# Kernel optimization log

Hardware: AMD Instinct MI355X
Metric: run time of the kernel (lower is better)

Reference implementation:

```python
import jax, jax.numpy as jnp
import numpy as np

EPS = 1e-5
DELTA = 0.2
VIS_LAM = 1.0


def setup_inputs() -> dict:
    key = jax.random.key(0)
    k1, k2, k3 = jax.random.split(key, 3)
    Na, Ns, Nb, Ne, D = 16, 32, 100, 12, 512
    vis_feats = jax.random.normal(k1, (Na * Ns * Nb, D), dtype=jnp.float32)
    word_feats = jax.random.normal(k2, (Na * Ne, D), dtype=jnp.float32)
    entities_length = jax.random.randint(k3, (Na,), 0, Ne).astype(jnp.int64)
    return {"vis_feats": vis_feats, "word_feats": word_feats,
            "entities_length": entities_length, "Nb": Nb}


def reference(vis_feats, word_feats, entities_length, Nb):
    Na = entities_length.shape[0]
    Ne = word_feats.shape[0] // Na
    Ns = vis_feats.shape[0] // (Na * Nb)
    D = vis_feats.shape[1]
    ent = entities_length

    div_vec = jnp.where(ent == 0, 1, ent).astype(vis_feats.dtype)      # (Na,)
    # pad mask: entity slot e is padding for action a if e >= ent[a]
    col_mask = jnp.arange(Ne)[None, :] >= ent[:, None]                 # (Na, Ne)

    # masked similarity: (Na*Ns*Nb, Na*Ne)
    S_ = vis_feats @ word_feats.T
    S_ = jnp.where(col_mask.reshape(-1)[None, :], 0.0, S_)

    # --- train-only visual consistency loss ---
    S_vt = S_.reshape(Na, Ns, Nb, Na, Ne)
    # diagonal over the two action axes: S_vis[i] = S_vt[i,:,:,i,:]
    S_vis = S_vt[jnp.arange(Na), :, :, jnp.arange(Na), :]              # (Na, Ns, Nb, Ne)
    S_vis_ng = jax.lax.stop_gradient(S_vis)                            # torch.no_grad block
    sim_scr = S_vis_ng.max(axis=2)                                     # (Na, Ns, Ne)
    maxind = jnp.argmax(S_vis_ng, axis=2)                              # (Na, Ns, Ne)
    smin = sim_scr.min(axis=1, keepdims=True)
    smax = sim_scr.max(axis=1, keepdims=True)
    sim_scr = ((sim_scr - smin) / (smax - smin + EPS))[..., None]      # (Na, Ns, Ne, 1)

    # NOTE: original code indexes vis_feats with the raw box index (< Nb);
    # reproduced faithfully.
    vcls = vis_feats[maxind.reshape(-1)].reshape(Na, Ns, Ne, D)
    vcls = vcls / (jnp.linalg.norm(vcls, axis=3, keepdims=True) + EPS)
    vcls = vcls * sim_scr
    v1 = vcls.transpose(0, 2, 1, 3)                                    # (Na, Ne, Ns, D)
    vis_mat = 1.0 - jnp.einsum('aesd,aetd->aest', v1, v1)              # (Na, Ne, Ns, Ns)
    eye = jnp.eye(Ns, dtype=bool)
    mvis = col_mask[:, :, None, None] | eye[None, None, :, :]
    vis_mat = jnp.where(mvis, 0.0, vis_mat)
    dem = jnp.count_nonzero(vis_mat).astype(vis_mat.dtype)
    vis_loss = vis_mat.sum() / dem

    # --- margin loss over frame-level scores ---
    S = S_.reshape(Na * Ns, Nb, Na * Ne).max(axis=1).reshape(Na, Ns, Na * Ne)
    Smin = S.min(axis=1, keepdims=True)
    Smax = S.max(axis=1, keepdims=True)
    S = S * ((S - Smin) / (Smax - Smin + EPS))
    Sf = S.reshape(Na, Ns, Na, Ne).sum(-1) / div_vec                   # (Na, Ns, Na)
    Sf_diag = Sf[jnp.arange(Na), :, jnp.arange(Na)]                    # (Na, Ns)
    term1 = jax.nn.relu(Sf - Sf_diag.T[None, :, :] + DELTA).mean(0).T  # (Na, Ns)
    term2 = jax.nn.relu(Sf - Sf_diag[:, :, None] + DELTA).mean(2)      # (Na, Ns)
    frame_score = term1 + term2
    margin_loss = (frame_score.mean() + VIS_LAM * vis_loss) * 10.0

    S_sim = S_.reshape(Na * Ns, Nb, Na * Ne)
    D_sim = S_sim.max(axis=1)
    D_ind = jnp.argmax(S_sim, axis=1)
    return (D_ind, D_sim, margin_loss)
```

## Files before the change

### kernel.cpp

```cpp
#include <hip/hip_runtime.h>
#include <math.h>

#define NA 16
#define NS 32
#define NB 100
#define NE 12
#define DD 512
#define NQ (NA*NS)
#define NC (NA*NE)
#define OUT_SIM_OFF (NQ*NC)
#define EPSF 1e-5f
#define DELTAF 0.2f
#define EPS_R 0.15f

#define WS_B_FOFF 12288

typedef _Float16 f16x8 __attribute__((ext_vector_type(8)));
typedef float f32x4 __attribute__((ext_vector_type(4)));

__global__ __launch_bounds__(64) void k0_conv(
    const float* __restrict__ word, float* __restrict__ ws)
{
    const int kcc = blockIdx.x / 12;
    const int nt  = blockIdx.x - kcc*12;
    const int l   = threadIdx.x;
    if (blockIdx.x == 0 && l < 2) ws[l] = 0.f;

    const int col = nt*16 + (l & 15);
    const int k   = kcc*32 + (l >> 4)*8;
    const float* src = word + (size_t)col*DD + k;
    float4 v0 = *(const float4*)(src);
    float4 v1 = *(const float4*)(src + 4);
    f16x8 hv;
    hv[0]=(_Float16)v0.x; hv[1]=(_Float16)v0.y; hv[2]=(_Float16)v0.z; hv[3]=(_Float16)v0.w;
    hv[4]=(_Float16)v1.x; hv[5]=(_Float16)v1.y; hv[6]=(_Float16)v1.z; hv[7]=(_Float16)v1.w;
    unsigned short* wsB = (unsigned short*)(ws + WS_B_FOFF);
    const int kc2 = kcc >> 1, ks = kcc & 1;
    *(f16x8*)&wsB[(size_t)(((kc2*12 + nt)*2 + ks)*512) + l*8] = hv;
}

__global__ __launch_bounds__(512, 4) void k1_mfma(
    const float* __restrict__ vis, const float* __restrict__ word,
    const unsigned short* __restrict__ wsB,
    const int* __restrict__ ent, float* __restrict__ out)
{
    __shared__ __align__(16) char pool[81920];
    unsigned short* Abuf = (unsigned short*)pool;
    unsigned short* Bbuf = (unsigned short*)(pool + 32768);
    float* part_v = (float*)pool;
    int*   part_i = (int*)(pool + 1536);
    float* colmax = (float*)(pool + 3072);
    int*   cnts   = (int*)(pool + 3840);
    int*   cand   = (int*)(pool + 4608);
    int*   flist  = (int*)(pool + 5376);
    int*   nflag  = (int*)(pool + 6144);

    const int t    = threadIdx.x;
    const int lane = t & 63;
    const int wid  = t >> 6;
    const int wm   = wid >> 2;
    const int wn   = wid & 3;
    const int q    = blockIdx.x;
    const float* visq = vis + (size_t)q * NB * DD;

    f32x4 acc[4][3];
    #pragma unroll
    for (int mi = 0; mi < 4; mi++)
        #pragma unroll
        for (int ni = 0; ni < 3; ni++) acc[mi][ni] = (f32x4)0.f;

    float4 ar[4];

    #define A_LOAD(kb)                                                         \
        {   int l_ = t & 63;                                                   \
            int row = ((t >> 6) << 4) + (l_ & 15);                             \
            ar[0] = make_float4(0.f,0.f,0.f,0.f); ar[1] = ar[0];               \
            ar[2] = ar[0]; ar[3] = ar[0];                                      \
            if (row < NB) {                                                    \
                const float* p_ = visq + (size_t)row*DD + (kb) + ((l_>>4)<<3); \
                ar[0] = *(const float4*)p_;                                    \
                ar[1] = *(const float4*)(p_ + 4);                              \
                ar[2] = *(const float4*)(p_ + 32);                             \
                ar[3] = *(const float4*)(p_ + 36); } }
    #define A_STORE(pn)                                                       \
        {   int mt_ = t >> 6;                                                 \
            f16x8 h0, h1;                                                     \
            h0[0]=(_Float16)ar[0].x; h0[1]=(_Float16)ar[0].y;                 \
            h0[2]=(_Float16)ar[0].z; h0[3]=(_Float16)ar[0].w;                 \
            h0[4]=(_Float16)ar[1].x; h0[5]=(_Float16)ar[1].y;                 \
            h0[6]=(_Float16)ar[1].z; h0[7]=(_Float16)ar[1].w;                 \
            h1[0]=(_Float16)ar[2].x; h1[1]=(_Float16)ar[2].y;                 \
            h1[2]=(_Float16)ar[2].z; h1[3]=(_Float16)ar[2].w;                 \
            h1[4]=(_Float16)ar[3].x; h1[5]=(_Float16)ar[3].y;                 \
            h1[6]=(_Float16)ar[3].z; h1[7]=(_Float16)ar[3].w;                 \
            *(f16x8*)&Abuf[(pn)*8192 + (mt_*2+0)*512 + (t&63)*8] = h0;        \
            *(f16x8*)&Abuf[(pn)*8192 + (mt_*2+1)*512 + (t&63)*8] = h1; }
    #define B_STAGE(kcn, pn)                                                   \
        {   const unsigned short* bsrc = wsB + (size_t)(kcn)*12288;            \
            unsigned short* bdst = Bbuf + (pn)*12288;                          \
            _Pragma("unroll")                                                  \
            for (int i = 0; i < 3; i++)                                        \
                __builtin_amdgcn_global_load_lds(                              \
                    (const void*)(bsrc + ((size_t)(i*512 + wid*64 + lane))*8), \
                    (void*)(bdst + (i*512 + wid*64)*8), 16, 0, 0); }

    {
        B_STAGE(0, 0);
        A_LOAD(0);
        A_STORE(0);
    }
    __syncthreads();

    for (int kc = 0; kc < 8; ++kc) {
        const int p = kc & 1;
        if (kc < 7) {
            A_LOAD((kc+1)*64);
            B_STAGE(kc+1, p^1);
        }
        {
            const unsigned short* Bp = Bbuf + p*12288;
            const unsigned short* Ap = Abuf + p*8192;
            #pragma unroll
            for (int ks = 0; ks < 2; ks++) {
                f16x8 bf[3];
                #pragma unroll
                for (int ni = 0; ni < 3; ni++)
                    bf[ni] = *((const f16x8*)&Bp[((wn*3 + ni)*2 + ks)*512 + lane*8]);
                #pragma unroll
                for (int mi = 0; mi < 4; mi++) {
                    f16x8 af = *((const f16x8*)&Ap[((wm*4 + mi)*2 + ks)*512 + lane*8]);
                    #pragma unroll
                    for (int ni = 0; ni < 3; ni++)
                        acc[mi][ni] = __builtin_amdgcn_mfma_f32_16x16x32_f16(af, bf[ni], acc[mi][ni], 0, 0, 0);
                }
            }
        }
        if (kc < 7) { A_STORE(p^1); }
        __syncthreads();
    }

    #pragma unroll
    for (int ni = 0; ni < 3; ni++) {
        float bv = -INFINITY; int bg = 1000;
        #pragma unroll
        for (int mi = 0; mi < 4; mi++)
            #pragma unroll
            for (int r = 0; r < 4; r++) {
                int g = wm*64 + mi*16 + ((lane>>4)<<2) + r;
                float v = acc[mi][ni][r];
                if (g < NB && (v > bv || (v == bv && g < bg))) { bv = v; bg = g; }
            }
        #pragma unroll
        for (int off = 16; off <= 32; off <<= 1) {
            float ov = __shfl_xor(bv, off);
            int   og = __shfl_xor(bg, off);
            if (ov > bv || (ov == bv && og < bg)) { bv = ov; bg = og; }
        }
        if (lane < 16) {
            int col = wn*48 + ni*16 + lane;
            part_v[wm*NC + col] = bv; part_i[wm*NC + col] = bg;
        }
    }
    if (t < NC) { cnts[t] = 0; cand[t] = 0; }
    if (t == 0) *nflag = 0;
    __syncthreads();

    float fbv = 0.f; int fbg = 0; bool fmask = true;
    if (t < NC) {
        fbv = part_v[t]; fbg = part_i[t];
        float v1 = part_v[NC + t]; int g1 = part_i[NC + t];
        if (v1 > fbv || (v1 == fbv && g1 < fbg)) { fbv = v1; fbg = g1; }
        int a2 = t / NE, e = t - a2*NE;
        fmask = (e >= ent[a2]);
        colmax[t] = fmask ? INFINITY : fbv;
    }
    __syncthreads();

    #pragma unroll
    for (int ni = 0; ni < 3; ni++) {
        int col = wn*48 + ni*16 + (lane & 15);
        float cm = colmax[col] - EPS_R;
        #pragma unroll
        for (int mi = 0; mi < 4; mi++)
            #pragma unroll
            for (int r = 0; r < 4; r++) {
                int g = wm*64 + mi*16 + ((lane>>4)<<2) + r;
                float v = acc[mi][ni][r];
                if (g < NB && v >= cm) {
                    int s = atomicAdd(&cnts[col], 1);
                    if (s < 3) atomicOr(&cand[col], (g + 1) << (8*s));
                }
            }
    }
    __syncthreads();

    if (t < NC) {
        if (fmask) {
            out[(size_t)q*NC + t] = 0.f;
            out[OUT_SIM_OFF + (size_t)q*NC + t] = 0.f;
        } else if (cnts[t] <= 1) {
            out[(size_t)q*NC + t] = (float)fbg;
            out[OUT_SIM_OFF + (size_t)q*NC + t] = fbv;
        } else {
            int idx = atomicAdd(nflag, 1);
            flist[idx] = t;
        }
    }
    __syncthreads();

    const int nf = *nflag;
    for (int f = wid; f < nf; f += 8) {
        int col = flist[f];
        int cnt = cnts[col];
        const float* wc = word + (size_t)col*DD;
        float bv; int bg;
        if (cnt <= 3) {
            int grp = lane >> 4, li = lane & 15;
            int cpk = cand[col];
            int myrow = (grp < cnt) ? (((cpk >> (8*grp)) & 255) - 1) : -1;
            float d = 0.f;
            if (myrow >= 0) {
                const float* vr = visq + (size_t)myrow*DD + li*32;
                const float* wb = wc + li*32;
                #pragma unroll
                for (int m = 0; m < 8; ++m) {
                    float4 a = *(const float4*)(vr + m*4);
                    float4 b = *(const float4*)(wb + m*4);
                    d = fmaf(a.x, b.x, d); d = fmaf(a.y, b.y, d);
                    d = fmaf(a.z, b.z, d); d = fmaf(a.w, b.w, d);
                }
            }
            #pragma unroll
            for (int off = 1; off <= 8; off <<= 1) d += __shfl_xor(d, off);
            float v0 = __shfl(d, 0), v1 = __shfl(d, 16), v2 = __shfl(d, 32);
            int r0 = ( cpk        & 255) - 1;
            int r1 = ((cpk >> 8)  & 255) - 1;
            int r2 = ((cpk >> 16) & 255) - 1;
            bv = v0; bg = r0;
            if (cnt >= 2 && (v1 > bv || (v1 == bv && r1 < bg))) { bv = v1; bg = r1; }
            if (cnt >= 3 && (v2 > bv || (v2 == bv && r2 < bg))) { bv = v2; bg = r2; }
        } else {
            float mbv = -INFINITY; int mbg = 1000;
            for (int r = lane; r < NB; r += 64) {
                float d = 0.f;
                const float* vr = visq + (size_t)r*DD;
                for (int m = 0; m < DD/4; ++m) {
                    float4 a = *(const float4*)(vr + m*4);
                    float4 b = *(const float4*)(wc + m*4);
                    d = fmaf(a.x, b.x, d); d = fmaf(a.y, b.y, d);
                    d = fmaf(a.z, b.z, d); d = fmaf(a.w, b.w, d);
                }
                if (d > mbv || (d == mbv && r < mbg)) { mbv = d; mbg = r; }
            }
            bv = mbv; bg = mbg;
            #pragma unroll
            for (int off = 32; off >= 1; off >>= 1) {
                float ov = __shfl_xor(bv, off); int og = __shfl_xor(bg, off);
                if (ov > bv || (ov == bv && og < bg)) { bv = ov; bg = og; }
            }
        }
        if (lane == 0) {
            out[(size_t)q*NC + col] = (float)bg;
            out[OUT_SIM_OFF + (size_t)q*NC + col] = bv;
        }
    }
}

__global__ __launch_bounds__(256) void k23_fused(
    const float* __restrict__ vis, const int* __restrict__ ent,
    const float* __restrict__ out_ro, float* __restrict__ ws)
{
    __shared__ __align__(16) char pool[74240];
    const int t = threadIdx.x;

    if (blockIdx.x < 192) {
        const int a = blockIdx.x / NE;
        const int e = blockIdx.x - a*NE;
        if (e >= ent[a]) return;

        float* VT   = (float*)pool;
        float* simv = (float*)(pool + 73728);
        int*   indv = (int*)(pool + 73856);
        float* scl  = (float*)(pool + 73984);
        float* wsum = (float*)(pool + 74112);
        float* wcnt = (float*)(pool + 74128);

        if (t < NS) {
            int q = a*NS + t;
            simv[t] = out_ro[OUT_SIM_OFF + (size_t)q*NC + a*NE + e];
            indv[t] = (int)out_ro[(size_t)q*NC + a*NE + e];
        }
        __syncthreads();
        if (t < NS) {
            float v = simv[t];
            float mn = v, mx = v;
            #pragma unroll
            for (int off = 16; off >= 1; off >>= 1) {
                mn = fminf(mn, __shfl_xor(mn, off));
                mx = fmaxf(mx, __shfl_xor(mx, off));
            }
            simv[t] = (v - mn) / (mx - mn + EPSF);
        }
        __syncthreads();

        const int g = t >> 3, j = t & 7;
        const float* src = vis + (size_t)indv[g]*DD;
        float ss = 0.f;
        #pragma unroll
        for (int i = 0; i < 16; i++) {
            int k4 = j + 8*i;
            float4 v = *(const float4*)(src + k4*4);
            ss = fmaf(v.x,v.x, fmaf(v.y,v.y, fmaf(v.z,v.z, fmaf(v.w,v.w, ss))));
            int k = k4*4;
            VT[(k+0)*36 + g] = v.x;
            VT[(k+1)*36 + g] = v.y;
            VT[(k+2)*36 + g] = v.z;
            VT[(k+3)*36 + g] = v.w;
        }
        #pragma unroll
        for (int off = 4; off >= 1; off >>= 1) ss += __shfl_xor(ss, off);
        if (j == 0) scl[g] = simv[g] / (sqrtf(ss) + EPSF);
        __syncthreads();

        const int s = t >> 3, tq = t & 7;
        float g0=0.f, g1=0.f, g2=0.f, g3=0.f;
        for (int k = 0; k < DD; k++) {
            float vs = VT[k*36 + s];
            float4 vt = *(const float4*)&VT[k*36 + tq*4];
            g0 = fmaf(vs, vt.x, g0);
            g1 = fmaf(vs, vt.y, g1);
            g2 = fmaf(vs, vt.z, g2);
            g3 = fmaf(vs, vt.w, g3);
        }
        float lsum = 0.f, lcnt = 0.f;
        float sc_s = scl[s];
        float gv[4] = {g0, g1, g2, g3};
        #pragma unroll
        for (int jj = 0; jj < 4; jj++) {
            int tt = tq*4 + jj;
            if (tt != s) {
                float val = 1.f - sc_s * scl[tt] * gv[jj];
                lsum += val;
                if (val != 0.f) lcnt += 1.f;
            }
        }
        #pragma unroll
        for (int off = 32; off >= 1; off >>= 1) {
            lsum += __shfl_xor(lsum, off);
            lcnt += __shfl_xor(lcnt, off);
        }
        const int wid = t >> 6, lane = t & 63;
        if (lane == 0) { wsum[wid] = lsum; wcnt[wid] = lcnt; }
        __syncthreads();
        if (t == 0) {
            atomicAdd(&ws[0], wsum[0]+wsum[1]+wsum[2]+wsum[3]);
            atomicAdd(&ws[1], wcnt[0]+wcnt[1]+wcnt[2]+wcnt[3]);
        }
    } else {
        const int a = blockIdx.x - 192;
        float* Ss  = (float*)pool;
        float* Smn = (float*)(pool + 24576);
        float* Smx = (float*)(pool + 25344);

        for (int e2 = t; e2 < NS*NC; e2 += 256) {
            int s = e2 / NC, c = e2 - (e2/NC)*NC;
            Ss[s*NC + c] = out_ro[OUT_SIM_OFF + (size_t)(a*NS + s)*NC + c];
        }
        __syncthreads();
        if (t < NC) {
            float mn = INFINITY, mx = -INFINITY;
            #pragma unroll
            for (int s = 0; s < NS; s++) {
                float v = Ss[s*NC + t];
                mn = fminf(mn, v); mx = fmaxf(mx, v);
            }
            Smn[t] = mn; Smx[t] = mx;
        }
        __syncthreads();
        for (int p = t; p < NS*NA; p += 256) {
            int s = p >> 4, b = p & 15;
            int eb = ent[b];
            float dv = (eb == 0) ? 1.f : (float)eb;
            float sum = 0.f;
            #pragma unroll
            for (int e2 = 0; e2 < NE; e2++) {
                int c = b*NE + e2;
                float S = Ss[s*NC + c];
                float r = (S - Smn[c]) / (Smx[c] - Smn[c] + EPSF);
                sum += S * r;
            }
            ws[2 + a*(NS*NA) + s*NA + b] = sum / dv;
        }
    }
}

__global__ __launch_bounds__(256) void k4_final(
    const float* __restrict__ ws_ro, float* __restrict__ out)
{
    __shared__ float Sf[NA][NS][NA];
    __shared__ float dg[NA][NS];
    __shared__ float wred[4];
    const int t = threadIdx.x;
    for (int e2 = t; e2 < NA*NS*NA; e2 += 256)
        ((float*)Sf)[e2] = ws_ro[2 + e2];
    __syncthreads();
    for (int p = t; p < NA*NS; p += 256) {
        int aa = p >> 5, s = p & 31;
        dg[aa][s] = Sf[aa][s][aa];
    }
    __syncthreads();
    float fsum = 0.f;
    for (int p = t; p < NA*NS; p += 256) {
        int i = p >> 5, s = p & 31;
        float d = dg[i][s];
        float t1 = 0.f, t2 = 0.f;
        #pragma unroll
        for (int x = 0; x < NA; x++) {
            t1 += fmaxf(Sf[x][s][i] - d + DELTAF, 0.f);
            t2 += fmaxf(Sf[i][s][x] - d + DELTAF, 0.f);
        }
        fsum += (t1 + t2) * (1.f/16.f);
    }
    #pragma unroll
    for (int off = 32; off >= 1; off >>= 1) fsum += __shfl_xor(fsum, off);
    const int wid = t >> 6, lane = t & 63;
    if (lane == 0) wred[wid] = fsum;
    __syncthreads();
    if (t == 0) {
        float frame_mean = (wred[0]+wred[1]+wred[2]+wred[3]) / 512.f;
        float vis_loss = ws_ro[0] / ws_ro[1];
        out[2*OUT_SIM_OFF] = (frame_mean + 1.0f * vis_loss) * 10.f;
    }
}

extern "C" void kernel_launch(void* const* d_in, const int* in_sizes, int n_in,
                              void* d_out, int out_size, void* d_ws, size_t ws_size,
                              hipStream_t stream)
{
    (void)in_sizes; (void)n_in; (void)out_size; (void)ws_size;
    const float* vis  = (const float*)d_in[0];
    const float* word = (const float*)d_in[1];
    const int*   ent  = (const int*)d_in[2];
    float* out = (float*)d_out;
    float* ws  = (float*)d_ws;
    const unsigned short* wsB = (const unsigned short*)(ws + WS_B_FOFF);

    k0_conv<<<192, 64, 0, stream>>>(word, ws);
    k1_mfma<<<NQ, 512, 0, stream>>>(vis, word, wsB, ent, out);
    k23_fused<<<208, 256, 0, stream>>>(vis, ent, out, ws);
    k4_final<<<1, 256, 0, stream>>>(ws, out);
}
```

Before: 56.89 us.

## Deepen GEMM A-prefetch pipeline and fold final reduction into last block

```diff
diff --git a/kernel.cpp b/kernel.cpp
--- a/kernel.cpp
+++ b/kernel.cpp
@@ -13,6 +13,7 @@
 #define DELTAF 0.2f
 #define EPS_R 0.15f
 
+#define WS_SF 16
 #define WS_B_FOFF 12288
 
 typedef _Float16 f16x8 __attribute__((ext_vector_type(8)));
@@ -24,7 +25,7 @@
     const int kcc = blockIdx.x / 12;
     const int nt  = blockIdx.x - kcc*12;
     const int l   = threadIdx.x;
-    if (blockIdx.x == 0 && l < 2) ws[l] = 0.f;
+    if (blockIdx.x == 0 && l < 3) ws[l] = 0.f;
 
     const int col = nt*16 + (l & 15);
     const int k   = kcc*32 + (l >> 4)*8;
@@ -69,30 +70,30 @@
         #pragma unroll
         for (int ni = 0; ni < 3; ni++) acc[mi][ni] = (f32x4)0.f;
 
-    float4 ar[4];
-
-    #define A_LOAD(kb)                                                         \
+    float4 arA[4], arB[4];
+
+    #define A_LOAD(dst, kb)                                                    \
         {   int l_ = t & 63;                                                   \
             int row = ((t >> 6) << 4) + (l_ & 15);                             \
-            ar[0] = make_float4(0.f,0.f,0.f,0.f); ar[1] = ar[0];               \
-            ar[2] = ar[0]; ar[3] = ar[0];                                      \
+            dst[0] = make_float4(0.f,0.f,0.f,0.f); dst[1] = dst[0];            \
+            dst[2] = dst[0]; dst[3] = dst[0];                                  \
             if (row < NB) {                                                    \
                 const float* p_ = visq + (size_t)row*DD + (kb) + ((l_>>4)<<3); \
-                ar[0] = *(const float4*)p_;                                    \
-                ar[1] = *(const float4*)(p_ + 4);                              \
-                ar[2] = *(const float4*)(p_ + 32);                             \
-                ar[3] = *(const float4*)(p_ + 36); } }
-    #define A_STORE(pn)                                                       \
+                dst[0] = *(const float4*)p_;                                   \
+                dst[1] = *(const float4*)(p_ + 4);                             \
+                dst[2] = *(const float4*)(p_ + 32);                            \
+                dst[3] = *(const float4*)(p_ + 36); } }
+    #define A_STORE(src, pn)                                                  \
         {   int mt_ = t >> 6;                                                 \
             f16x8 h0, h1;                                                     \
-            h0[0]=(_Float16)ar[0].x; h0[1]=(_Float16)ar[0].y;                 \
-            h0[2]=(_Float16)ar[0].z; h0[3]=(_Float16)ar[0].w;                 \
-            h0[4]=(_Float16)ar[1].x; h0[5]=(_Float16)ar[1].y;                 \
-            h0[6]=(_Float16)ar[1].z; h0[7]=(_Float16)ar[1].w;                 \
-            h1[0]=(_Float16)ar[2].x; h1[1]=(_Float16)ar[2].y;                 \
-            h1[2]=(_Float16)ar[2].z; h1[3]=(_Float16)ar[2].w;                 \
-            h1[4]=(_Float16)ar[3].x; h1[5]=(_Float16)ar[3].y;                 \
-            h1[6]=(_Float16)ar[3].z; h1[7]=(_Float16)ar[3].w;                 \
+            h0[0]=(_Float16)src[0].x; h0[1]=(_Float16)src[0].y;               \
+            h0[2]=(_Float16)src[0].z; h0[3]=(_Float16)src[0].w;               \
+            h0[4]=(_Float16)src[1].x; h0[5]=(_Float16)src[1].y;               \
+            h0[6]=(_Float16)src[1].z; h0[7]=(_Float16)src[1].w;               \
+            h1[0]=(_Float16)src[2].x; h1[1]=(_Float16)src[2].y;               \
+            h1[2]=(_Float16)src[2].z; h1[3]=(_Float16)src[2].w;               \
+            h1[4]=(_Float16)src[3].x; h1[5]=(_Float16)src[3].y;               \
+            h1[6]=(_Float16)src[3].z; h1[7]=(_Float16)src[3].w;               \
             *(f16x8*)&Abuf[(pn)*8192 + (mt_*2+0)*512 + (t&63)*8] = h0;        \
             *(f16x8*)&Abuf[(pn)*8192 + (mt_*2+1)*512 + (t&63)*8] = h1; }
     #define B_STAGE(kcn, pn)                                                   \
@@ -104,18 +105,26 @@
                     (const void*)(bsrc + ((size_t)(i*512 + wid*64 + lane))*8), \
                     (void*)(bdst + (i*512 + wid*64)*8), 16, 0, 0); }
 
-    {
-        B_STAGE(0, 0);
-        A_LOAD(0);
-        A_STORE(0);
-    }
-    __syncthreads();
+    A_LOAD(arA, 0);
+    B_STAGE(0, 0);
+    A_LOAD(arB, 64);
+    A_STORE(arA, 0);
+    asm volatile("s_waitcnt vmcnt(4) lgkmcnt(0)" ::: "memory");
+    __builtin_amdgcn_sched_barrier(0);
+    __builtin_amdgcn_s_barrier();
+    __builtin_amdgcn_sched_barrier(0);
 
     for (int kc = 0; kc < 8; ++kc) {
         const int p = kc & 1;
         if (kc < 7) {
-            A_LOAD((kc+1)*64);
+            if ((kc & 1) == 0) { A_STORE(arB, p^1); } else { A_STORE(arA, p^1); }
             B_STAGE(kc+1, p^1);
+            __builtin_amdgcn_sched_barrier(0);
+            if (kc < 6) {
+                if ((kc & 1) == 0) { A_LOAD(arA, (kc+2)*64); }
+                else               { A_LOAD(arB, (kc+2)*64); }
+            }
+            __builtin_amdgcn_sched_barrier(0);
         }
         {
             const unsigned short* Bp = Bbuf + p*12288;
@@ -135,9 +144,17 @@
                 }
             }
         }
-        if (kc < 7) { A_STORE(p^1); }
-        __syncthreads();
-    }
+        if (kc < 7) {
+            if (kc < 6)
+                asm volatile("s_waitcnt vmcnt(4) lgkmcnt(0)" ::: "memory");
+            else
+                asm volatile("s_waitcnt vmcnt(0) lgkmcnt(0)" ::: "memory");
+            __builtin_amdgcn_sched_barrier(0);
+            __builtin_amdgcn_s_barrier();
+            __builtin_amdgcn_sched_barrier(0);
+        }
+    }
+    __syncthreads();
 
     #pragma unroll
     for (int ni = 0; ni < 3; ni++) {
@@ -268,93 +285,94 @@
 
 __global__ __launch_bounds__(256) void k23_fused(
     const float* __restrict__ vis, const int* __restrict__ ent,
-    const float* __restrict__ out_ro, float* __restrict__ ws)
+    const float* __restrict__ out_ro, float* ws, float* out)
 {
     __shared__ __align__(16) char pool[74240];
+    __shared__ int lastFlag;
     const int t = threadIdx.x;
 
     if (blockIdx.x < 192) {
         const int a = blockIdx.x / NE;
         const int e = blockIdx.x - a*NE;
-        if (e >= ent[a]) return;
-
-        float* VT   = (float*)pool;
-        float* simv = (float*)(pool + 73728);
-        int*   indv = (int*)(pool + 73856);
-        float* scl  = (float*)(pool + 73984);
-        float* wsum = (float*)(pool + 74112);
-        float* wcnt = (float*)(pool + 74128);
-
-        if (t < NS) {
-            int q = a*NS + t;
-            simv[t] = out_ro[OUT_SIM_OFF + (size_t)q*NC + a*NE + e];
-            indv[t] = (int)out_ro[(size_t)q*NC + a*NE + e];
-        }
-        __syncthreads();
-        if (t < NS) {
-            float v = simv[t];
-            float mn = v, mx = v;
-            #pragma unroll
-            for (int off = 16; off >= 1; off >>= 1) {
-                mn = fminf(mn, __shfl_xor(mn, off));
-                mx = fmaxf(mx, __shfl_xor(mx, off));
-            }
-            simv[t] = (v - mn) / (mx - mn + EPSF);
-        }
-        __syncthreads();
-
-        const int g = t >> 3, j = t & 7;
-        const float* src = vis + (size_t)indv[g]*DD;
-        float ss = 0.f;
-        #pragma unroll
-        for (int i = 0; i < 16; i++) {
-            int k4 = j + 8*i;
-            float4 v = *(const float4*)(src + k4*4);
-            ss = fmaf(v.x,v.x, fmaf(v.y,v.y, fmaf(v.z,v.z, fmaf(v.w,v.w, ss))));
-            int k = k4*4;
-            VT[(k+0)*36 + g] = v.x;
-            VT[(k+1)*36 + g] = v.y;
-            VT[(k+2)*36 + g] = v.z;
-            VT[(k+3)*36 + g] = v.w;
-        }
-        #pragma unroll
-        for (int off = 4; off >= 1; off >>= 1) ss += __shfl_xor(ss, off);
-        if (j == 0) scl[g] = simv[g] / (sqrtf(ss) + EPSF);
-        __syncthreads();
-
-        const int s = t >> 3, tq = t & 7;
-        float g0=0.f, g1=0.f, g2=0.f, g3=0.f;
-        for (int k = 0; k < DD; k++) {
-            float vs = VT[k*36 + s];
-            float4 vt = *(const float4*)&VT[k*36 + tq*4];
-            g0 = fmaf(vs, vt.x, g0);
-            g1 = fmaf(vs, vt.y, g1);
-            g2 = fmaf(vs, vt.z, g2);
-            g3 = fmaf(vs, vt.w, g3);
-        }
-        float lsum = 0.f, lcnt = 0.f;
-        float sc_s = scl[s];
-        float gv[4] = {g0, g1, g2, g3};
-        #pragma unroll
-        for (int jj = 0; jj < 4; jj++) {
-            int tt = tq*4 + jj;
-            if (tt != s) {
-                float val = 1.f - sc_s * scl[tt] * gv[jj];
-                lsum += val;
-                if (val != 0.f) lcnt += 1.f;
-            }
-        }
-        #pragma unroll
-        for (int off = 32; off >= 1; off >>= 1) {
-            lsum += __shfl_xor(lsum, off);
-            lcnt += __shfl_xor(lcnt, off);
-        }
-        const int wid = t >> 6, lane = t & 63;
-        if (lane == 0) { wsum[wid] = lsum; wcnt[wid] = lcnt; }
-        __syncthreads();
-        if (t == 0) {
-            atomicAdd(&ws[0], wsum[0]+wsum[1]+wsum[2]+wsum[3]);
-            atomicAdd(&ws[1], wcnt[0]+wcnt[1]+wcnt[2]+wcnt[3]);
+        if (e < ent[a]) {
+            float* VT   = (float*)pool;
+            float* simv = (float*)(pool + 73728);
+            int*   indv = (int*)(pool + 73856);
+            float* scl  = (float*)(pool + 73984);
+            float* wsum = (float*)(pool + 74112);
+            float* wcnt = (float*)(pool + 74128);
+
+            if (t < NS) {
+                int q = a*NS + t;
+                simv[t] = out_ro[OUT_SIM_OFF + (size_t)q*NC + a*NE + e];
+                indv[t] = (int)out_ro[(size_t)q*NC + a*NE + e];
+            }
+            __syncthreads();
+            if (t < NS) {
+                float v = simv[t];
+                float mn = v, mx = v;
+                #pragma unroll
+                for (int off = 16; off >= 1; off >>= 1) {
+                    mn = fminf(mn, __shfl_xor(mn, off));
+                    mx = fmaxf(mx, __shfl_xor(mx, off));
+                }
+                simv[t] = (v - mn) / (mx - mn + EPSF);
+            }
+            __syncthreads();
+
+            const int g = t >> 3, j = t & 7;
+            const float* src = vis + (size_t)indv[g]*DD;
+            float ss = 0.f;
+            #pragma unroll
+            for (int i = 0; i < 16; i++) {
+                int k4 = j + 8*i;
+                float4 v = *(const float4*)(src + k4*4);
+                ss = fmaf(v.x,v.x, fmaf(v.y,v.y, fmaf(v.z,v.z, fmaf(v.w,v.w, ss))));
+                int k = k4*4;
+                VT[(k+0)*36 + g] = v.x;
+                VT[(k+1)*36 + g] = v.y;
+                VT[(k+2)*36 + g] = v.z;
+                VT[(k+3)*36 + g] = v.w;
+            }
+            #pragma unroll
+            for (int off = 4; off >= 1; off >>= 1) ss += __shfl_xor(ss, off);
+            if (j == 0) scl[g] = simv[g] / (sqrtf(ss) + EPSF);
+            __syncthreads();
+
+            const int s = t >> 3, tq = t & 7;
+            float g0=0.f, g1=0.f, g2=0.f, g3=0.f;
+            for (int k = 0; k < DD; k++) {
+                float vs = VT[k*36 + s];
+                float4 vt = *(const float4*)&VT[k*36 + tq*4];
+                g0 = fmaf(vs, vt.x, g0);
+                g1 = fmaf(vs, vt.y, g1);
+                g2 = fmaf(vs, vt.z, g2);
+                g3 = fmaf(vs, vt.w, g3);
+            }
+            float lsum = 0.f, lcnt = 0.f;
+            float sc_s = scl[s];
+            float gv[4] = {g0, g1, g2, g3};
+            #pragma unroll
+            for (int jj = 0; jj < 4; jj++) {
+                int tt = tq*4 + jj;
+                if (tt != s) {
+                    float val = 1.f - sc_s * scl[tt] * gv[jj];
+                    lsum += val;
+                    if (val != 0.f) lcnt += 1.f;
+                }
+            }
+            #pragma unroll
+            for (int off = 32; off >= 1; off >>= 1) {
+                lsum += __shfl_xor(lsum, off);
+                lcnt += __shfl_xor(lcnt, off);
+            }
+            const int wid = t >> 6, lane = t & 63;
+            if (lane == 0) { wsum[wid] = lsum; wcnt[wid] = lcnt; }
+            __syncthreads();
+            if (t == 0) {
+                atomicAdd(&ws[0], wsum[0]+wsum[1]+wsum[2]+wsum[3]);
+                atomicAdd(&ws[1], wcnt[0]+wcnt[1]+wcnt[2]+wcnt[3]);
+            }
         }
     } else {
         const int a = blockIdx.x - 192;
@@ -389,47 +407,51 @@
                 float r = (S - Smn[c]) / (Smx[c] - Smn[c] + EPSF);
                 sum += S * r;
             }
-            ws[2 + a*(NS*NA) + s*NA + b] = sum / dv;
-        }
-    }
-}
-
-__global__ __launch_bounds__(256) void k4_final(
-    const float* __restrict__ ws_ro, float* __restrict__ out)
-{
-    __shared__ float Sf[NA][NS][NA];
-    __shared__ float dg[NA][NS];
-    __shared__ float wred[4];
-    const int t = threadIdx.x;
-    for (int e2 = t; e2 < NA*NS*NA; e2 += 256)
-        ((float*)Sf)[e2] = ws_ro[2 + e2];
-    __syncthreads();
-    for (int p = t; p < NA*NS; p += 256) {
-        int aa = p >> 5, s = p & 31;
-        dg[aa][s] = Sf[aa][s][aa];
-    }
-    __syncthreads();
-    float fsum = 0.f;
-    for (int p = t; p < NA*NS; p += 256) {
-        int i = p >> 5, s = p & 31;
-        float d = dg[i][s];
-        float t1 = 0.f, t2 = 0.f;
+            ws[WS_SF + a*(NS*NA) + s*NA + b] = sum / dv;
+        }
+    }
+
+    __threadfence();
+    if (t == 0) {
+        unsigned old = atomicAdd((unsigned int*)(ws + 2), 1u);
+        lastFlag = (old == 207u) ? 1 : 0;
+    }
+    __syncthreads();
+    if (lastFlag) {
+        __threadfence();
+        float* Sf   = (float*)pool;
+        float* dg   = (float*)(pool + 32768);
+        float* wred = (float*)(pool + 34816);
+        for (int e2 = t; e2 < NA*NS*NA; e2 += 256)
+            Sf[e2] = ws[WS_SF + e2];
+        __syncthreads();
+        for (int p = t; p < NA*NS; p += 256) {
+            int aa = p >> 5, s = p & 31;
+            dg[aa*NS + s] = Sf[(aa*NS + s)*NA + aa];
+        }
+        __syncthreads();
+        float fsum = 0.f;
+        for (int p = t; p < NA*NS; p += 256) {
+            int i = p >> 5, s = p & 31;
+            float d = dg[i*NS + s];
+            float t1 = 0.f, t2 = 0.f;
+            #pragma unroll
+            for (int x = 0; x < NA; x++) {
+                t1 += fmaxf(Sf[(x*NS + s)*NA + i] - d + DELTAF, 0.f);
+                t2 += fmaxf(Sf[(i*NS + s)*NA + x] - d + DELTAF, 0.f);
+            }
+            fsum += (t1 + t2) * (1.f/16.f);
+        }
         #pragma unroll
-        for (int x = 0; x < NA; x++) {
-            t1 += fmaxf(Sf[x][s][i] - d + DELTAF, 0.f);
-            t2 += fmaxf(Sf[i][s][x] - d + DELTAF, 0.f);
-        }
-        fsum += (t1 + t2) * (1.f/16.f);
-    }
-    #pragma unroll
-    for (int off = 32; off >= 1; off >>= 1) fsum += __shfl_xor(fsum, off);
-    const int wid = t >> 6, lane = t & 63;
-    if (lane == 0) wred[wid] = fsum;
-    __syncthreads();
-    if (t == 0) {
-        float frame_mean = (wred[0]+wred[1]+wred[2]+wred[3]) / 512.f;
-        float vis_loss = ws_ro[0] / ws_ro[1];
-        out[2*OUT_SIM_OFF] = (frame_mean + 1.0f * vis_loss) * 10.f;
+        for (int off = 32; off >= 1; off >>= 1) fsum += __shfl_xor(fsum, off);
+        const int wid = t >> 6, lane = t & 63;
+        if (lane == 0) wred[wid] = fsum;
+        __syncthreads();
+        if (t == 0) {
+            float frame_mean = (wred[0]+wred[1]+wred[2]+wred[3]) / 512.f;
+            float vis_loss = ws[0] / ws[1];
+            out[2*OUT_SIM_OFF] = (frame_mean + 1.0f * vis_loss) * 10.f;
+        }
     }
 }
 
@@ -447,6 +469,5 @@
 
     k0_conv<<<192, 64, 0, stream>>>(word, ws);
     k1_mfma<<<NQ, 512, 0, stream>>>(vis, word, wsB, ent, out);
-    k23_fused<<<208, 256, 0, stream>>>(vis, ent, out, ws);
-    k4_final<<<1, 256, 0, stream>>>(ws, out);
+    k23_fused<<<208, 256, 0, stream>>>(vis, ent, out, ws, out);
 }
```

Result: slower. 66.95 us (+17.7%).

## Load A fragments directly into registers and give each wave all columns

Applied to the files above, without the earlier changes.

```diff
diff --git a/kernel.cpp b/kernel.cpp
--- a/kernel.cpp
+++ b/kernel.cpp
@@ -44,112 +44,92 @@
     const unsigned short* __restrict__ wsB,
     const int* __restrict__ ent, float* __restrict__ out)
 {
-    __shared__ __align__(16) char pool[81920];
-    unsigned short* Abuf = (unsigned short*)pool;
-    unsigned short* Bbuf = (unsigned short*)(pool + 32768);
+    __shared__ __align__(16) char pool[49152];
+    unsigned short* Bbuf = (unsigned short*)pool;
     float* part_v = (float*)pool;
-    int*   part_i = (int*)(pool + 1536);
-    float* colmax = (float*)(pool + 3072);
-    int*   cnts   = (int*)(pool + 3840);
-    int*   cand   = (int*)(pool + 4608);
-    int*   flist  = (int*)(pool + 5376);
-    int*   nflag  = (int*)(pool + 6144);
+    int*   part_i = (int*)(pool + 6144);
+    float* colmax = (float*)(pool + 12288);
+    int*   cnts   = (int*)(pool + 13056);
+    int*   cand   = (int*)(pool + 13824);
+    int*   flist  = (int*)(pool + 14592);
+    int*   nflag  = (int*)(pool + 15360);
 
     const int t    = threadIdx.x;
     const int lane = t & 63;
-    const int wid  = t >> 6;
-    const int wm   = wid >> 2;
-    const int wn   = wid & 3;
+    const int w    = t >> 6;
     const int q    = blockIdx.x;
     const float* visq = vis + (size_t)q * NB * DD;
 
-    f32x4 acc[4][3];
+    f32x4 acc[12];
     #pragma unroll
-    for (int mi = 0; mi < 4; mi++)
-        #pragma unroll
-        for (int ni = 0; ni < 3; ni++) acc[mi][ni] = (f32x4)0.f;
-
-    float4 ar[4];
-
-    #define A_LOAD(kb)                                                         \
-        {   int l_ = t & 63;                                                   \
-            int row = ((t >> 6) << 4) + (l_ & 15);                             \
-            ar[0] = make_float4(0.f,0.f,0.f,0.f); ar[1] = ar[0];               \
-            ar[2] = ar[0]; ar[3] = ar[0];                                      \
-            if (row < NB) {                                                    \
-                const float* p_ = visq + (size_t)row*DD + (kb) + ((l_>>4)<<3); \
-                ar[0] = *(const float4*)p_;                                    \
-                ar[1] = *(const float4*)(p_ + 4);                              \
-                ar[2] = *(const float4*)(p_ + 32);                             \
-                ar[3] = *(const float4*)(p_ + 36); } }
-    #define A_STORE(pn)                                                       \
-        {   int mt_ = t >> 6;                                                 \
-            f16x8 h0, h1;                                                     \
-            h0[0]=(_Float16)ar[0].x; h0[1]=(_Float16)ar[0].y;                 \
-            h0[2]=(_Float16)ar[0].z; h0[3]=(_Float16)ar[0].w;                 \
-            h0[4]=(_Float16)ar[1].x; h0[5]=(_Float16)ar[1].y;                 \
-            h0[6]=(_Float16)ar[1].z; h0[7]=(_Float16)ar[1].w;                 \
-            h1[0]=(_Float16)ar[2].x; h1[1]=(_Float16)ar[2].y;                 \
-            h1[2]=(_Float16)ar[2].z; h1[3]=(_Float16)ar[2].w;                 \
-            h1[4]=(_Float16)ar[3].x; h1[5]=(_Float16)ar[3].y;                 \
-            h1[6]=(_Float16)ar[3].z; h1[7]=(_Float16)ar[3].w;                 \
-            *(f16x8*)&Abuf[(pn)*8192 + (mt_*2+0)*512 + (t&63)*8] = h0;        \
-            *(f16x8*)&Abuf[(pn)*8192 + (mt_*2+1)*512 + (t&63)*8] = h1; }
+    for (int nt = 0; nt < 12; nt++) acc[nt] = (f32x4)0.f;
+
+    int arow = w*16 + (lane & 15);
+    const float* aptr = visq + (size_t)(arow < NB ? arow : 0)*DD + ((lane >> 4) << 3);
+
     #define B_STAGE(kcn, pn)                                                   \
         {   const unsigned short* bsrc = wsB + (size_t)(kcn)*12288;            \
             unsigned short* bdst = Bbuf + (pn)*12288;                          \
             _Pragma("unroll")                                                  \
             for (int i = 0; i < 3; i++)                                        \
                 __builtin_amdgcn_global_load_lds(                              \
-                    (const void*)(bsrc + ((size_t)(i*512 + wid*64 + lane))*8), \
-                    (void*)(bdst + (i*512 + wid*64)*8), 16, 0, 0); }
-
+                    (const void*)(bsrc + ((size_t)(i*512 + w*64 + lane))*8),   \
+                    (void*)(bdst + (i*512 + w*64)*8), 16, 0, 0); }
+
+    float4 ar[2][4];
+
+    B_STAGE(0, 0);
     {
-        B_STAGE(0, 0);
-        A_LOAD(0);
-        A_STORE(0);
-    }
-    __syncthreads();
-
+        const float* p_ = aptr;
+        ar[0][0] = *(const float4*)(p_);
+        ar[0][1] = *(const float4*)(p_ + 4);
+        ar[0][2] = *(const float4*)(p_ + 32);
+        ar[0][3] = *(const float4*)(p_ + 36);
+    }
+    __syncthreads();
+
+    #pragma unroll
     for (int kc = 0; kc < 8; ++kc) {
         const int p = kc & 1;
         if (kc < 7) {
-            A_LOAD((kc+1)*64);
             B_STAGE(kc+1, p^1);
-        }
+            const float* p_ = aptr + (kc+1)*64;
+            ar[p^1][0] = *(const float4*)(p_);
+            ar[p^1][1] = *(const float4*)(p_ + 4);
+            ar[p^1][2] = *(const float4*)(p_ + 32);
+            ar[p^1][3] = *(const float4*)(p_ + 36);
+        }
+        f16x8 af0, af1;
+        af0[0]=(_Float16)ar[p][0].x; af0[1]=(_Float16)ar[p][0].y;
+        af0[2]=(_Float16)ar[p][0].z; af0[3]=(_Float16)ar[p][0].w;
+        af0[4]=(_Float16)ar[p][1].x; af0[5]=(_Float16)ar[p][1].y;
+        af0[6]=(_Float16)ar[p][1].z; af0[7]=(_Float16)ar[p][1].w;
+        af1[0]=(_Float16)ar[p][2].x; af1[1]=(_Float16)ar[p][2].y;
+        af1[2]=(_Float16)ar[p][2].z; af1[3]=(_Float16)ar[p][2].w;
+        af1[4]=(_Float16)ar[p][3].x; af1[5]=(_Float16)ar[p][3].y;
+        af1[6]=(_Float16)ar[p][3].z; af1[7]=(_Float16)ar[p][3].w;
         {
             const unsigned short* Bp = Bbuf + p*12288;
-            const unsigned short* Ap = Abuf + p*8192;
-            #pragma unroll
-            for (int ks = 0; ks < 2; ks++) {
-                f16x8 bf[3];
-                #pragma unroll
-                for (int ni = 0; ni < 3; ni++)
-                    bf[ni] = *((const f16x8*)&Bp[((wn*3 + ni)*2 + ks)*512 + lane*8]);
-                #pragma unroll
-                for (int mi = 0; mi < 4; mi++) {
-                    f16x8 af = *((const f16x8*)&Ap[((wm*4 + mi)*2 + ks)*512 + lane*8]);
-                    #pragma unroll
-                    for (int ni = 0; ni < 3; ni++)
-                        acc[mi][ni] = __builtin_amdgcn_mfma_f32_16x16x32_f16(af, bf[ni], acc[mi][ni], 0, 0, 0);
-                }
-            }
-        }
-        if (kc < 7) { A_STORE(p^1); }
+            #pragma unroll
+            for (int nt = 0; nt < 12; nt++) {
+                f16x8 bf0 = *((const f16x8*)&Bp[(nt*2+0)*512 + lane*8]);
+                f16x8 bf1 = *((const f16x8*)&Bp[(nt*2+1)*512 + lane*8]);
+                acc[nt] = __builtin_amdgcn_mfma_f32_16x16x32_f16(af0, bf0, acc[nt], 0, 0, 0);
+                acc[nt] = __builtin_amdgcn_mfma_f32_16x16x32_f16(af1, bf1, acc[nt], 0, 0, 0);
+            }
+        }
         __syncthreads();
     }
 
     #pragma unroll
-    for (int ni = 0; ni < 3; ni++) {
+    for (int nt = 0; nt < 12; nt++) {
         float bv = -INFINITY; int bg = 1000;
         #pragma unroll
-        for (int mi = 0; mi < 4; mi++)
-            #pragma unroll
-            for (int r = 0; r < 4; r++) {
-                int g = wm*64 + mi*16 + ((lane>>4)<<2) + r;
-                float v = acc[mi][ni][r];
-                if (g < NB && (v > bv || (v == bv && g < bg))) { bv = v; bg = g; }
-            }
+        for (int r = 0; r < 4; r++) {
+            int g = w*16 + ((lane>>4)<<2) + r;
+            float v = acc[nt][r];
+            if (g < NB && (v > bv || (v == bv && g < bg))) { bv = v; bg = g; }
+        }
         #pragma unroll
         for (int off = 16; off <= 32; off <<= 1) {
             float ov = __shfl_xor(bv, off);
@@ -157,8 +137,8 @@
             if (ov > bv || (ov == bv && og < bg)) { bv = ov; bg = og; }
         }
         if (lane < 16) {
-            int col = wn*48 + ni*16 + lane;
-            part_v[wm*NC + col] = bv; part_i[wm*NC + col] = bg;
+            part_v[w*NC + nt*16 + lane] = bv;
+            part_i[w*NC + nt*16 + lane] = bg;
         }
     }
     if (t < NC) { cnts[t] = 0; cand[t] = 0; }
@@ -167,9 +147,12 @@
 
     float fbv = 0.f; int fbg = 0; bool fmask = true;
     if (t < NC) {
-        fbv = part_v[t]; fbg = part_i[t];
-        float v1 = part_v[NC + t]; int g1 = part_i[NC + t];
-        if (v1 > fbv || (v1 == fbv && g1 < fbg)) { fbv = v1; fbg = g1; }
+        fbv = -INFINITY; fbg = 1000;
+        #pragma unroll
+        for (int ww = 0; ww < 8; ww++) {
+            float v = part_v[ww*NC + t]; int g = part_i[ww*NC + t];
+            if (v > fbv || (v == fbv && g < fbg)) { fbv = v; fbg = g; }
+        }
         int a2 = t / NE, e = t - a2*NE;
         fmask = (e >= ent[a2]);
         colmax[t] = fmask ? INFINITY : fbv;
@@ -177,20 +160,18 @@
     __syncthreads();
 
     #pragma unroll
-    for (int ni = 0; ni < 3; ni++) {
-        int col = wn*48 + ni*16 + (lane & 15);
+    for (int nt = 0; nt < 12; nt++) {
+        int col = nt*16 + (lane & 15);
         float cm = colmax[col] - EPS_R;
         #pragma unroll
-        for (int mi = 0; mi < 4; mi++)
-            #pragma unroll
-            for (int r = 0; r < 4; r++) {
-                int g = wm*64 + mi*16 + ((lane>>4)<<2) + r;
-                float v = acc[mi][ni][r];
-                if (g < NB && v >= cm) {
-                    int s = atomicAdd(&cnts[col], 1);
-                    if (s < 3) atomicOr(&cand[col], (g + 1) << (8*s));
-                }
-            }
+        for (int r = 0; r < 4; r++) {
+            int g = w*16 + ((lane>>4)<<2) + r;
+            float v = acc[nt][r];
+            if (g < NB && v >= cm) {
+                int s = atomicAdd(&cnts[col], 1);
+                if (s < 3) atomicOr(&cand[col], (g + 1) << (8*s));
+            }
+        }
     }
     __syncthreads();
 
@@ -209,7 +190,7 @@
     __syncthreads();
 
     const int nf = *nflag;
-    for (int f = wid; f < nf; f += 8) {
+    for (int f = w; f < nf; f += 8) {
         int col = flist[f];
         int cnt = cnts[col];
         const float* wc = word + (size_t)col*DD;
```

Result: slower. 59.33 us (+4.3%).
